# Performance work log

Measured on AMD Instinct MI355X. Metric: run time of the kernel, lower is better.

The kernel has to match this reference:

```python
import jax, jax.numpy as jnp
import numpy as np

B, T, E = 2, 2048, 1024
H, D = 16, 64
FF = 4096
EPS = 1e-5


def _layer_norm(x, g, b):
    m = jnp.mean(x, axis=-1, keepdims=True)
    v = jnp.mean(jnp.square(x - m), axis=-1, keepdims=True)
    return (x - m) * jax.lax.rsqrt(v + EPS) * g + b


def setup_inputs() -> dict:
    key = jax.random.key(0)
    ks = jax.random.split(key, 8)
    s = lambda fan_in: 1.0 / np.sqrt(fan_in)
    return {
        "src": jax.random.normal(ks[0], (B, T, E), jnp.float32),
        "Wq": jax.random.normal(ks[1], (E, E), jnp.float32) * s(E),
        "Wk": jax.random.normal(ks[2], (E, E), jnp.float32) * s(E),
        "Wv": jax.random.normal(ks[3], (E, E), jnp.float32) * s(E),
        "Wo": jax.random.normal(ks[4], (E, E), jnp.float32) * s(E),
        "W1": jax.random.normal(ks[5], (2 * FF, E), jnp.float32) * s(E),
        "b1": jnp.zeros((2 * FF,), jnp.float32),
        "W2": jax.random.normal(ks[6], (E, FF), jnp.float32) * s(FF),
        "b2": jnp.zeros((E,), jnp.float32),
        "ln1_w": jnp.ones((E,), jnp.float32),
        "ln1_b": jnp.zeros((E,), jnp.float32),
        "ln2_w": jnp.ones((E,), jnp.float32),
        "ln2_b": jnp.zeros((E,), jnp.float32),
    }


def reference(src, Wq, Wk, Wv, Wo, W1, b1, W2, b2, ln1_w, ln1_b, ln2_w, ln2_b):
    # --- pre-norm self-attention block ---
    h = _layer_norm(src, ln1_w, ln1_b)                       # [B,T,E]
    q = (h @ Wq.T).reshape(B, T, H, D)                       # [B,T,H,D]
    k = (h @ Wk.T).reshape(B, T, H, D)
    v = (h @ Wv.T).reshape(B, T, H, D)
    scores = jnp.einsum("bqhd,bkhd->bhqk", q, k) / np.sqrt(D)
    probs = jax.nn.softmax(scores, axis=-1)                  # [B,H,T,T]
    attn = jnp.einsum("bhqk,bkhd->bqhd", probs, v).reshape(B, T, E)
    x = src + attn @ Wo.T                                    # residual (dropout=0)
    # --- pre-norm GEGLU FFN block ---
    h2 = _layer_norm(x, ln2_w, ln2_b)
    u = h2 @ W1.T + b1                                       # [B,T,2*FF]
    a, gates = jnp.split(u, 2, axis=-1)
    f = a * jax.nn.gelu(gates, approximate=False)            # GEGLU (exact erf gelu)
    return x + (f @ W2.T + b2)
```

## Files before the change

### kernel.cpp

```cpp
#include <hip/hip_runtime.h>
#include <stdint.h>
#include <math.h>

#define DEVI __device__ __forceinline__

typedef __attribute__((ext_vector_type(8))) short sv8;
typedef __attribute__((ext_vector_type(4))) short sv4;
typedef __attribute__((ext_vector_type(4))) float fv4;

typedef __attribute__((address_space(1))) void av1_t;
typedef __attribute__((address_space(3))) void av3_t;

constexpr int Bb = 2, Tt = 2048, Ee = 1024, Hh = 16, Dd = 64, FFd = 4096;
constexpr int NN = Bb * Tt;
constexpr float EPSv = 1e-5f;

#define WAIT_VM(n) asm volatile("s_waitcnt vmcnt(" #n ")" ::: "memory")
#define LGKM0 asm volatile("s_waitcnt lgkmcnt(0)" ::: "memory")

DEVI float b2f(unsigned short s) {
  union { unsigned u; float f; } v; v.u = ((unsigned)s) << 16; return v.f;
}
DEVI unsigned short f2b(float f) {
  union { float f; unsigned u; } v; v.f = f;
  return (unsigned short)((v.u + 0x7FFFu + ((v.u >> 16) & 1u)) >> 16);
}
DEVI unsigned short f2b_rtz(float f) {
  union { float f; unsigned u; } v; v.f = f;
  return (unsigned short)(v.u >> 16);
}

DEVI void load_lds16(const void* g, void* s) {
  __builtin_amdgcn_global_load_lds((av1_t*)(unsigned long long)g,
                                   (av3_t*)(unsigned)(unsigned long long)s,
                                   16, 0, 0);
}

__global__ __launch_bounds__(256) void cvt_all_kernel(
    const float* __restrict__ Wq, const float* __restrict__ Wk,
    const float* __restrict__ Wv, const float* __restrict__ Wo,
    const float* __restrict__ W1, const float* __restrict__ W2,
    unsigned short* __restrict__ wqkv, unsigned short* __restrict__ wo16,
    unsigned short* __restrict__ w116, unsigned short* __restrict__ w216,
    float s2) {
  const int bid = blockIdx.x;
  if (bid < 4096) {
    const int wsel = bid >> 10;
    const int i = ((bid & 1023) * 256 + threadIdx.x) * 4;
    const float* src = (wsel == 0) ? Wq : (wsel == 1) ? Wk : (wsel == 2) ? Wv : Wo;
    unsigned short* dst = (wsel == 3) ? wo16 : (wqkv + (size_t)wsel * Ee * Ee);
    const float sc = (wsel == 0) ? s2 : 1.0f;
    const float4 v = *(const float4*)(src + i);
    sv4 o;
    o[0] = (short)f2b(v.x * sc); o[1] = (short)f2b(v.y * sc);
    o[2] = (short)f2b(v.z * sc); o[3] = (short)f2b(v.w * sc);
    *(sv4*)(dst + i) = o;
  } else if (bid < 12288) {
    const int i = ((bid - 4096) * 256 + threadIdx.x) * 4;
    const int r = i >> 10, c = i & 1023;
    const int rp = (r < FFd) ? ((r >> 4) * 32 + (r & 15))
                             : (((r - FFd) >> 4) * 32 + 16 + (r & 15));
    const float4 v = *(const float4*)(W1 + i);
    sv4 o;
    o[0] = (short)f2b(v.x); o[1] = (short)f2b(v.y);
    o[2] = (short)f2b(v.z); o[3] = (short)f2b(v.w);
    *(sv4*)(w116 + (size_t)rp * Ee + c) = o;
  } else {
    const int i = ((bid - 12288) * 256 + threadIdx.x) * 4;
    const float4 v = *(const float4*)(W2 + i);
    sv4 o;
    o[0] = (short)f2b(v.x); o[1] = (short)f2b(v.y);
    o[2] = (short)f2b(v.z); o[3] = (short)f2b(v.w);
    *(sv4*)(w216 + i) = o;
  }
}

__global__ __launch_bounds__(256) void vt_kernel(const unsigned short* __restrict__ qkv,
                                                 unsigned short* __restrict__ vT) {
  const int bh = blockIdx.y;
  const int b = bh >> 4, h = bh & 15;
  const int tt = blockIdx.x * 64;
  const int tid = threadIdx.x;
  __shared__ unsigned short tile[64][65];
  const int tr = tid >> 2, tc4 = (tid & 3) * 16;
  const unsigned short* src = qkv + (size_t)(b * Tt + tt + tr) * (3 * Ee) + 2 * Ee + h * 64 + tc4;
  const sv8 a0 = *(const sv8*)src;
  const sv8 a1 = *(const sv8*)(src + 8);
#pragma unroll
  for (int j = 0; j < 8; ++j) { tile[tr][tc4 + j] = a0[j]; tile[tr][tc4 + 8 + j] = a1[j]; }
  __syncthreads();
  unsigned short* dst = vT + ((size_t)bh * 64 + tr) * Tt + tt + tc4;
  sv8 o0, o1;
#pragma unroll
  for (int j = 0; j < 8; ++j) { o0[j] = (short)tile[tc4 + j][tr]; o1[j] = (short)tile[tc4 + 8 + j][tr]; }
  *(sv8*)dst = o0;
  *(sv8*)(dst + 8) = o1;
}

__global__ __launch_bounds__(256) void ln_kernel(const float* __restrict__ x,
                                                 const float* __restrict__ g,
                                                 const float* __restrict__ b,
                                                 unsigned short* __restrict__ out) {
  const int row = blockIdx.x, tid = threadIdx.x;
  const float4 v = *(const float4*)(x + (size_t)row * Ee + tid * 4);
  float s = v.x + v.y + v.z + v.w;
  float ss = v.x * v.x + v.y * v.y + v.z * v.z + v.w * v.w;
#pragma unroll
  for (int off = 32; off; off >>= 1) { s += __shfl_down(s, off); ss += __shfl_down(ss, off); }
  __shared__ float red[16];
  const int w = tid >> 6, l = tid & 63;
  if (l == 0) { red[w] = s; red[8 + w] = ss; }
  __syncthreads();
  s = red[0] + red[1] + red[2] + red[3];
  ss = red[8] + red[9] + red[10] + red[11];
  const float mean = s * (1.f / Ee);
  const float rstd = rsqrtf(ss * (1.f / Ee) - mean * mean + EPSv);
  const float4 gv = *(const float4*)(g + tid * 4);
  const float4 bv = *(const float4*)(b + tid * 4);
  sv4 o;
  o[0] = (short)f2b((v.x - mean) * rstd * gv.x + bv.x);
  o[1] = (short)f2b((v.y - mean) * rstd * gv.y + bv.y);
  o[2] = (short)f2b((v.z - mean) * rstd * gv.z + bv.z);
  o[3] = (short)f2b((v.w - mean) * rstd * gv.w + bv.w);
  *(sv4*)(out + (size_t)row * Ee + tid * 4) = o;
}

template <int OUTF32, int HASBIAS, int BN, int GEGLU>
__global__ __launch_bounds__(256) void gemm_bt(const unsigned short* __restrict__ A,
                                               const unsigned short* __restrict__ Bw,
                                               void* __restrict__ Cout,
                                               const float* __restrict__ bias,
                                               const float* __restrict__ res,
                                               int M, int K) {
  constexpr int NI = BN / 32;
  __shared__ unsigned short lA[3][128 * 32];
  __shared__ unsigned short lB[3][BN * 32];
  const int tid = threadIdx.x;
  const int l = tid & 63, w = tid >> 6;
  const int wr = w >> 1, wc = w & 1;
  const int rowbase = blockIdx.y * 128, colbase = blockIdx.x * BN;

  const fv4 zero4 = {0.f, 0.f, 0.f, 0.f};
  fv4 acc[4][NI];
#pragma unroll
  for (int i = 0; i < 4; ++i)
#pragma unroll
    for (int j = 0; j < NI; ++j) acc[i][j] = zero4;

  const int c0 = tid, c1 = tid + 256;
  const int sw0 = ((c0 & 3) ^ ((c0 >> 3) & 3)) * 8;
  const int sw1 = ((c1 & 3) ^ ((c1 >> 3) & 3)) * 8;
  const unsigned short* Ag0 = A + (size_t)(rowbase + (c0 >> 2)) * K + sw0;
  const unsigned short* Ag1 = A + (size_t)(rowbase + (c1 >> 2)) * K + sw1;
  const unsigned short* Bg0 = Bw + (size_t)(colbase + (c0 >> 2)) * K + sw0;
  const unsigned short* Bg1 = Bw + (size_t)(colbase + ((BN == 128 ? c1 : c0) >> 2)) * K +
                              (BN == 128 ? sw1 : sw0);

  const int nk = K >> 5;

  auto stage = [&](int buf) {
    load_lds16(Ag0, lA[buf] + c0 * 8);
    load_lds16(Ag1, lA[buf] + c1 * 8);
    load_lds16(Bg0, lB[buf] + c0 * 8);
    if (BN == 128) load_lds16(Bg1, lB[buf] + c1 * 8);
    Ag0 += 32; Ag1 += 32; Bg0 += 32; Bg1 += 32;
  };

  stage(0);
  stage(1);
  if constexpr (BN == 128) WAIT_VM(4); else WAIT_VM(3);
  __builtin_amdgcn_s_barrier();

  int cur = 0;
  for (int t = 0; t < nk; ++t) {
    const int pf = (cur + 2 >= 3) ? cur - 1 : cur + 2;
    if (t + 2 < nk) stage(pf);
    sv8 af[4], bfr[NI];
#pragma unroll
    for (int i = 0; i < 4; ++i) {
      const int ra = wr * 64 + i * 16 + (l & 15);
      af[i] = *(const sv8*)(lA[cur] + ra * 32 + (((l >> 4) ^ ((ra >> 1) & 3)) * 8));
    }
#pragma unroll
    for (int i = 0; i < NI; ++i) {
      const int rb = wc * (BN / 2) + i * 16 + (l & 15);
      bfr[i] = *(const sv8*)(lB[cur] + rb * 32 + (((l >> 4) ^ ((rb >> 1) & 3)) * 8));
    }
    __builtin_amdgcn_s_setprio(1);
#pragma unroll
    for (int mi = 0; mi < 4; ++mi)
#pragma unroll
      for (int ni = 0; ni < NI; ++ni)
        acc[mi][ni] = __builtin_amdgcn_mfma_f32_16x16x32_bf16(af[mi], bfr[ni], acc[mi][ni], 0, 0, 0);
    __builtin_amdgcn_s_setprio(0);
    if (t + 2 < nk) {
      if constexpr (BN == 128) WAIT_VM(4); else WAIT_VM(3);
      __builtin_amdgcn_s_barrier();
    } else if (t + 1 < nk) {
      WAIT_VM(0);
      __builtin_amdgcn_s_barrier();
    }
    cur = (cur + 1 >= 3) ? 0 : cur + 1;
  }

  const int r0 = rowbase + wr * 64 + ((l >> 4) * 4);
  const int ccol = colbase + wc * (BN / 2) + (l & 15);
#pragma unroll
  for (int mi = 0; mi < 4; ++mi) {
#pragma unroll
    for (int j = 0; j < 4; ++j) {
      const size_t r = (size_t)(r0 + mi * 16 + j);
      if (GEGLU) {
#pragma unroll
        for (int p = 0; p < NI / 2; ++p) {
          const int ca = ccol + p * 32;
          const int ocol = ((ca >> 5) << 4) | (ca & 15);
          const float av = acc[mi][2 * p][j] + bias[ocol];
          const float gv = acc[mi][2 * p + 1][j] + bias[ocol + (M >> 1)];
          const float y = 0.7978845608028654f * (gv + 0.044715f * gv * gv * gv);
          const float e = exp2f(2.8853900817779268f * y);
          const float gel = gv * (1.f - 1.f / (e + 1.f));
          ((unsigned short*)Cout)[r * (size_t)(M >> 1) + ocol] = f2b(av * gel);
        }
      } else {
#pragma unroll
        for (int ni = 0; ni < NI; ++ni) {
          const int c = ccol + ni * 16;
          float vv = acc[mi][ni][j];
          if (HASBIAS) vv += bias[c];
          if (OUTF32) {
            ((float*)Cout)[r * M + c] = res[r * M + c] + vv;
          } else {
            ((unsigned short*)Cout)[r * M + c] = f2b(vv);
          }
        }
      }
    }
  }
}

template <int GEGLU>
__global__ __launch_bounds__(512, 2) void gemm256(const unsigned short* __restrict__ A,
                                                  const unsigned short* __restrict__ Bw,
                                                  void* __restrict__ Cout,
                                                  const float* __restrict__ bias,
                                                  int M, int K) {
  __shared__ unsigned short Ah[2][2][256 * 32];
  __shared__ unsigned short Bh[2][2][256 * 32];
  const int tid = threadIdx.x;
  const int l = tid & 63, w = tid >> 6;
  const int wrow = w >> 2, wcol = w & 3;
  const int nbase = blockIdx.y * 256, mbase = blockIdx.x * 256;

  const fv4 zero4 = {0.f, 0.f, 0.f, 0.f};
  fv4 acc[8][4];
#pragma unroll
  for (int i = 0; i < 8; ++i)
#pragma unroll
    for (int j = 0; j < 4; ++j) acc[i][j] = zero4;

  const int s0 = tid, s1 = tid + 512;
  const int r0 = s0 >> 2, x0 = (((s0 & 3) ^ ((r0 >> 1) & 3))) * 8;
  const int r1 = s1 >> 2, x1 = (((s1 & 3) ^ ((r1 >> 1) & 3))) * 8;
  const unsigned short* As0 = A + (size_t)(nbase + r0) * K + x0;
  const unsigned short* As1 = A + (size_t)(nbase + r1) * K + x1;
  const unsigned short* Bs0 = Bw + (size_t)(mbase + r0) * K + x0;
  const unsigned short* Bs1 = Bw + (size_t)(mbase + r1) * K + x1;

  const int nk = K >> 6;

  auto stA = [&](int db, int kh, int kof) {
    load_lds16(As0 + kof + kh * 32, &Ah[db][kh][s0 * 8]);
    load_lds16(As1 + kof + kh * 32, &Ah[db][kh][s1 * 8]);
  };
  auto stB = [&](int db, int kh, int kof) {
    load_lds16(Bs0 + kof + kh * 32, &Bh[db][kh][s0 * 8]);
    load_lds16(Bs1 + kof + kh * 32, &Bh[db][kh][s1 * 8]);
  };

  const int cl = (((l >> 4) ^ ((l >> 1) & 3))) * 8;
  const int arl = (wrow * 128 + (l & 15)) * 32 + cl;
  const int brl = (wcol * 64 + (l & 15)) * 32 + cl;

  stA(0, 0, 0); stB(0, 0, 0); stA(0, 1, 0); stB(0, 1, 0);

  for (int t = 0; t < nk; ++t) {
    const int st = t & 1, sf = st ^ 1;
    const int kof = (t + 1) * 64;
    const bool pre = (t + 1 < nk);
    sv8 af[8], b0, b1;

    WAIT_VM(4);
    __builtin_amdgcn_s_barrier();
    __builtin_amdgcn_sched_barrier(0);
    if (pre) stA(sf, 0, kof);
#pragma unroll
    for (int mi = 0; mi < 8; ++mi) af[mi] = *(const sv8*)(&Ah[st][0][arl + mi * 512]);
    b0 = *(const sv8*)(&Bh[st][0][brl]);
    b1 = *(const sv8*)(&Bh[st][0][brl + 512]);
    __builtin_amdgcn_s_setprio(1);
#pragma unroll
    for (int mi = 0; mi < 8; ++mi) {
      acc[mi][0] = __builtin_amdgcn_mfma_f32_16x16x32_bf16(af[mi], b0, acc[mi][0], 0, 0, 0);
      acc[mi][1] = __builtin_amdgcn_mfma_f32_16x16x32_bf16(af[mi], b1, acc[mi][1], 0, 0, 0);
    }
    __builtin_amdgcn_s_setprio(0);

    if (pre) stB(sf, 0, kof);
    b0 = *(const sv8*)(&Bh[st][0][brl + 2 * 512]);
    b1 = *(const sv8*)(&Bh[st][0][brl + 3 * 512]);
    __builtin_amdgcn_s_setprio(1);
#pragma unroll
    for (int mi = 0; mi < 8; ++mi) {
      acc[mi][2] = __builtin_amdgcn_mfma_f32_16x16x32_bf16(af[mi], b0, acc[mi][2], 0, 0, 0);
      acc[mi][3] = __builtin_amdgcn_mfma_f32_16x16x32_bf16(af[mi], b1, acc[mi][3], 0, 0, 0);
    }
    __builtin_amdgcn_s_setprio(0);

    if (pre) { WAIT_VM(4); } else { WAIT_VM(0); }
    __builtin_amdgcn_s_barrier();
    __builtin_amdgcn_sched_barrier(0);
    if (pre) stA(sf, 1, kof);
#pragma unroll
    for (int mi = 0; mi < 8; ++mi) af[mi] = *(const sv8*)(&Ah[st][1][arl + mi * 512]);
    b0 = *(const sv8*)(&Bh[st][1][brl]);
    b1 = *(const sv8*)(&Bh[st][1][brl + 512]);
    __builtin_amdgcn_s_setprio(1);
#pragma unroll
    for (int mi = 0; mi < 8; ++mi) {
      acc[mi][0] = __builtin_amdgcn_mfma_f32_16x16x32_bf16(af[mi], b0, acc[mi][0], 0, 0, 0);
      acc[mi][1] = __builtin_amdgcn_mfma_f32_16x16x32_bf16(af[mi], b1, acc[mi][1], 0, 0, 0);
    }
    __builtin_amdgcn_s_setprio(0);

    if (pre) stB(sf, 1, kof);
    b0 = *(const sv8*)(&Bh[st][1][brl + 2 * 512]);
    b1 = *(const sv8*)(&Bh[st][1][brl + 3 * 512]);
    __builtin_amdgcn_s_setprio(1);
#pragma unroll
    for (int mi = 0; mi < 8; ++mi) {
      acc[mi][2] = __builtin_amdgcn_mfma_f32_16x16x32_bf16(af[mi], b0, acc[mi][2], 0, 0, 0);
      acc[mi][3] = __builtin_amdgcn_mfma_f32_16x16x32_bf16(af[mi], b1, acc[mi][3], 0, 0, 0);
    }
    __builtin_amdgcn_s_setprio(0);
  }

  const int rbase = nbase + wrow * 128 + ((l >> 4) * 4);
  const int cbase = mbase + wcol * 64 + (l & 15);
#pragma unroll
  for (int mi = 0; mi < 8; ++mi) {
#pragma unroll
    for (int j = 0; j < 4; ++j) {
      const size_t r = (size_t)(rbase + mi * 16 + j);
      if (GEGLU) {
#pragma unroll
        for (int p = 0; p < 2; ++p) {
          const int ca = cbase + p * 32;
          const int ocol = ((ca >> 5) << 4) | (ca & 15);
          const float av = acc[mi][2 * p][j] + bias[ocol];
          const float gv = acc[mi][2 * p + 1][j] + bias[ocol + (M >> 1)];
          const float y = 0.7978845608028654f * (gv + 0.044715f * gv * gv * gv);
          const float e = exp2f(2.8853900817779268f * y);
          const float gel = gv * (1.f - 1.f / (e + 1.f));
          ((unsigned short*)Cout)[r * (size_t)(M >> 1) + ocol] = f2b(av * gel);
        }
      } else {
#pragma unroll
        for (int ni = 0; ni < 4; ++ni) {
          const int c = cbase + ni * 16;
          ((unsigned short*)Cout)[r * (size_t)M + c] = f2b(acc[mi][ni][j]);
        }
      }
    }
  }
}

__global__ __launch_bounds__(256) void attn_kernel(const unsigned short* __restrict__ Q,
                                                   const unsigned short* __restrict__ Kb,
                                                   const unsigned short* __restrict__ vT,
                                                   unsigned short* __restrict__ O,
                                                   int ld) {
  const int bidl = ((blockIdx.x & 7) << 7) + (blockIdx.x >> 3);
  const int bh = bidl >> 5;
  const int b = bh / Hh, h = bh % Hh;
  const int q0 = (bidl & 31) * 64;
  const int tid = threadIdx.x, l = tid & 63, w = tid >> 6;
  const size_t base = (size_t)b * Tt * ld + (size_t)h * Dd;
  const size_t baseO = (size_t)b * Tt * Ee + (size_t)h * Dd;
  const unsigned short* vTb = vT + (size_t)bh * 64 * Tt;

  __shared__ unsigned short Kt[2][64 * 64];
  __shared__ unsigned short Vt[2][64 * 64];
  __shared__ unsigned short Pt[4][16 * 64];

  sv8 qf0, qf1;
  {
    const unsigned short* qp = Q + base + (size_t)(q0 + w * 16 + (l & 15)) * ld + (l >> 4) * 8;
    qf0 = *(const sv8*)qp;
    qf1 = *(const sv8*)(qp + 32);
  }

  const fv4 zero4 = {0.f, 0.f, 0.f, 0.f};
  fv4 acc_o[4];
#pragma unroll
  for (int i = 0; i < 4; ++i) acc_o[i] = zero4;
  float Mx = -INFINITY;
  float Lp[4];
#pragma unroll
  for (int j = 0; j < 4; ++j) Lp[j] = 0.f;

  const int c0 = tid, c1 = tid + 256;
  const int r0c = c0 >> 3, xc0 = c0 & 7;
  const int r1c = c1 >> 3, xc1 = c1 & 7;

  load_lds16(Kb + base + (size_t)(r0c)*ld + (xc0 ^ (r0c & 7)) * 8, Kt[0] + c0 * 8);
  load_lds16(Kb + base + (size_t)(r1c)*ld + (xc1 ^ (r1c & 7)) * 8, Kt[0] + c1 * 8);
  load_lds16(vTb + (size_t)(r0c)*Tt + (xc0 ^ (r0c & 7)) * 8, Vt[0] + c0 * 8);
  load_lds16(vTb + (size_t)(r1c)*Tt + (xc1 ^ (r1c & 7)) * 8, Vt[0] + c1 * 8);
  __syncthreads();

  int cur = 0;
  for (int kt = 0; kt < Tt / 64; ++kt) {
    const int nx = cur ^ 1;
    if (kt + 1 < Tt / 64) {
      load_lds16(Kb + base + (size_t)((kt + 1) * 64 + r0c) * ld + (xc0 ^ (r0c & 7)) * 8, Kt[nx] + c0 * 8);
      load_lds16(Kb + base + (size_t)((kt + 1) * 64 + r1c) * ld + (xc1 ^ (r1c & 7)) * 8, Kt[nx] + c1 * 8);
      load_lds16(vTb + (size_t)(r0c)*Tt + (kt + 1) * 64 + (xc0 ^ (r0c & 7)) * 8, Vt[nx] + c0 * 8);
      load_lds16(vTb + (size_t)(r1c)*Tt + (kt + 1) * 64 + (xc1 ^ (r1c & 7)) * 8, Vt[nx] + c1 * 8);
    }

    fv4 s[4];
    __builtin_amdgcn_s_setprio(1);
#pragma unroll
    for (int ks = 0; ks < 4; ++ks) {
      const int row = ks * 16 + (l & 15);
      const sv8 kf0 = *(const sv8*)(Kt[cur] + row * 64 + (((l >> 4) ^ (row & 7)) * 8));
      const sv8 kf1 = *(const sv8*)(Kt[cur] + row * 64 + (((4 + (l >> 4)) ^ (row & 7)) * 8));
      fv4 t = zero4;
      t = __builtin_amdgcn_mfma_f32_16x16x32_bf16(qf0, kf0, t, 0, 0, 0);
      t = __builtin_amdgcn_mfma_f32_16x16x32_bf16(qf1, kf1, t, 0, 0, 0);
      s[ks] = t;
    }
    __builtin_amdgcn_s_setprio(0);

    float m01 = fmaxf(fmaxf(s[0][0], s[0][1]), fmaxf(s[0][2], s[0][3]));
    float m1 = fmaxf(fmaxf(s[1][0], s[1][1]), fmaxf(s[1][2], s[1][3]));
    float m2 = fmaxf(fmaxf(s[2][0], s[2][1]), fmaxf(s[2][2], s[2][3]));
    float m3 = fmaxf(fmaxf(s[3][0], s[3][1]), fmaxf(s[3][2], s[3][3]));
    float tm = fmaxf(fmaxf(m01, m1), fmaxf(m2, m3));
    if (__any(tm > Mx + 11.5f)) {
      float mt = tm;
#pragma unroll
      for (int off = 1; off < 16; off <<= 1) mt = fmaxf(mt, __shfl_xor(mt, off, 16));
      const float mnew = fmaxf(Mx, mt);
      const float alpha = exp2f(Mx - mnew);
      Mx = mnew;
#pragma unroll
      for (int j = 0; j < 4; ++j) {
        Lp[j] *= alpha;
#pragma unroll
        for (int dsb = 0; dsb < 4; ++dsb) acc_o[dsb][j] *= alpha;
      }
    }
#pragma unroll
    for (int ks = 0; ks < 4; ++ks)
#pragma unroll
      for (int j = 0; j < 4; ++j) {
        const float p = exp2f(s[ks][j] - Mx);
        s[ks][j] = p;
        Lp[j] += p;
      }
#pragma unroll
    for (int ks = 0; ks < 4; ++ks)
#pragma unroll
      for (int j = 0; j < 4; ++j) {
        const int q = (l >> 4) * 4 + j, k = ks * 16 + (l & 15);
        Pt[w][q * 64 + ((((k >> 3) ^ (q & 7)) & 7) * 8) + (k & 7)] = f2b_rtz(s[ks][j]);
      }
    LGKM0;

    __builtin_amdgcn_s_setprio(1);
#pragma unroll
    for (int kcn = 0; kcn < 2; ++kcn) {
      const int qr = l & 15;
      const sv8 pf = *(const sv8*)(&Pt[w][qr * 64 + (((kcn * 4 + (l >> 4)) ^ (qr & 7)) * 8)]);
#pragma unroll
      for (int dsb = 0; dsb < 4; ++dsb) {
        const int row = dsb * 16 + (l & 15);
        const int chunk = kcn * 4 + (l >> 4);
        const sv8 vf = *(const sv8*)(Vt[cur] + row * 64 + ((chunk ^ (row & 7)) * 8));
        acc_o[dsb] = __builtin_amdgcn_mfma_f32_16x16x32_bf16(pf, vf, acc_o[dsb], 0, 0, 0);
      }
    }
    __builtin_amdgcn_s_setprio(0);

    __syncthreads();
    cur = nx;
  }

#pragma unroll
  for (int j = 0; j < 4; ++j) {
    float t = Lp[j];
#pragma unroll
    for (int off = 1; off < 16; off <<= 1) t += __shfl_xor(t, off, 16);
    const float inv = 1.f / t;
    unsigned short* op = O + baseO + (size_t)(q0 + w * 16 + (l >> 4) * 4 + j) * Ee;
#pragma unroll
    for (int dsb = 0; dsb < 4; ++dsb)
      op[dsb * 16 + (l & 15)] = f2b(acc_o[dsb][j] * inv);
  }
}

extern "C" void kernel_launch(void* const* d_in, const int* in_sizes, int n_in,
                              void* d_out, int out_size, void* d_ws, size_t ws_size,
                              hipStream_t stream) {
  (void)in_sizes; (void)n_in; (void)out_size; (void)ws_size;
  const float* src  = (const float*)d_in[0];
  const float* Wq   = (const float*)d_in[1];
  const float* Wk   = (const float*)d_in[2];
  const float* Wv   = (const float*)d_in[3];
  const float* Wo   = (const float*)d_in[4];
  const float* W1   = (const float*)d_in[5];
  const float* b1   = (const float*)d_in[6];
  const float* W2   = (const float*)d_in[7];
  const float* b2   = (const float*)d_in[8];
  const float* ln1w = (const float*)d_in[9];
  const float* ln1b = (const float*)d_in[10];
  const float* ln2w = (const float*)d_in[11];
  const float* ln2b = (const float*)d_in[12];
  float* out = (float*)d_out;

  char* ws = (char*)d_ws;
  size_t off = 0;
  auto alloc = [&](size_t bytes) { char* p = ws + off; off += bytes; return p; };
  unsigned short* wqkv = (unsigned short*)alloc((size_t)3 * Ee * Ee * 2);
  unsigned short* wo16 = (unsigned short*)alloc((size_t)Ee * Ee * 2);
  unsigned short* w116 = (unsigned short*)alloc((size_t)2 * FFd * Ee * 2);
  unsigned short* w216 = (unsigned short*)alloc((size_t)Ee * FFd * 2);
  unsigned short* h16  = (unsigned short*)alloc((size_t)NN * Ee * 2);
  unsigned short* qkv  = (unsigned short*)alloc((size_t)NN * 3 * Ee * 2);
  unsigned short* a16  = (unsigned short*)alloc((size_t)NN * Ee * 2);
  float* xbuf          = (float*)alloc((size_t)NN * Ee * 4);
  unsigned short* vT   = (unsigned short*)alloc((size_t)NN * Ee * 2);
  unsigned short* f16  = qkv;

  const float s2 = 0.125f * 1.4426950408889634f;

  dim3 blk(256);
  cvt_all_kernel<<<dim3(16384), blk, 0, stream>>>(Wq, Wk, Wv, Wo, W1, W2,
                                                  wqkv, wo16, w116, w216, s2);

  ln_kernel<<<dim3(NN), blk, 0, stream>>>(src, ln1w, ln1b, h16);

  gemm_bt<0, 0, 128, 0><<<dim3(3 * Ee / 128, NN / 128), blk, 0, stream>>>(h16, wqkv, qkv, nullptr, nullptr, 3 * Ee, Ee);

  vt_kernel<<<dim3(Tt / 64, Bb * Hh), blk, 0, stream>>>(qkv, vT);

  attn_kernel<<<dim3(1024), blk, 0, stream>>>(qkv, qkv + Ee, vT, a16, 3 * Ee);

  gemm_bt<1, 0, 64, 0><<<dim3(Ee / 64, NN / 128), blk, 0, stream>>>(a16, wo16, xbuf, nullptr, src, Ee, Ee);

  ln_kernel<<<dim3(NN), blk, 0, stream>>>(xbuf, ln2w, ln2b, h16);

  gemm256<1><<<dim3(2 * FFd / 256, NN / 256), dim3(512), 0, stream>>>(h16, w116, f16, b1, 2 * FFd, Ee);

  gemm_bt<1, 1, 64, 0><<<dim3(Ee / 64, NN / 128), blk, 0, stream>>>(f16, w216, out, b2, xbuf, Ee, FFd);
}
```

Before: 292.5 us.

## Shrink GEGLU GEMM tile to 256x128 with triple-buffered 32-wide K pipeline

```diff
diff --git a/kernel.cpp b/kernel.cpp
--- a/kernel.cpp
+++ b/kernel.cpp
@@ -240,64 +240,58 @@
 }
 
 template <int GEGLU>
-__global__ __launch_bounds__(512, 2) void gemm256(const unsigned short* __restrict__ A,
+__global__ __launch_bounds__(512, 4) void gemm256(const unsigned short* __restrict__ A,
                                                   const unsigned short* __restrict__ Bw,
                                                   void* __restrict__ Cout,
                                                   const float* __restrict__ bias,
                                                   int M, int K) {
-  __shared__ unsigned short Ah[2][2][256 * 32];
-  __shared__ unsigned short Bh[2][2][256 * 32];
+  __shared__ unsigned short Ah[3][256 * 32];
+  __shared__ unsigned short Bh[3][128 * 32];
   const int tid = threadIdx.x;
   const int l = tid & 63, w = tid >> 6;
   const int wrow = w >> 2, wcol = w & 3;
-  const int nbase = blockIdx.y * 256, mbase = blockIdx.x * 256;
+  const int nbase = blockIdx.y * 256, mbase = blockIdx.x * 128;
 
   const fv4 zero4 = {0.f, 0.f, 0.f, 0.f};
-  fv4 acc[8][4];
-#pragma unroll
-  for (int i = 0; i < 8; ++i)
-#pragma unroll
-    for (int j = 0; j < 4; ++j) acc[i][j] = zero4;
-
-  const int s0 = tid, s1 = tid + 512;
-  const int r0 = s0 >> 2, x0 = (((s0 & 3) ^ ((r0 >> 1) & 3))) * 8;
-  const int r1 = s1 >> 2, x1 = (((s1 & 3) ^ ((r1 >> 1) & 3))) * 8;
-  const unsigned short* As0 = A + (size_t)(nbase + r0) * K + x0;
-  const unsigned short* As1 = A + (size_t)(nbase + r1) * K + x1;
-  const unsigned short* Bs0 = Bw + (size_t)(mbase + r0) * K + x0;
-  const unsigned short* Bs1 = Bw + (size_t)(mbase + r1) * K + x1;
-
-  const int nk = K >> 6;
-
-  auto stA = [&](int db, int kh, int kof) {
-    load_lds16(As0 + kof + kh * 32, &Ah[db][kh][s0 * 8]);
-    load_lds16(As1 + kof + kh * 32, &Ah[db][kh][s1 * 8]);
-  };
-  auto stB = [&](int db, int kh, int kof) {
-    load_lds16(Bs0 + kof + kh * 32, &Bh[db][kh][s0 * 8]);
-    load_lds16(Bs1 + kof + kh * 32, &Bh[db][kh][s1 * 8]);
+  fv4 acc[8][2];
+#pragma unroll
+  for (int i = 0; i < 8; ++i) { acc[i][0] = zero4; acc[i][1] = zero4; }
+
+  const int sA0 = tid, sA1 = tid + 512;
+  const int rA0 = sA0 >> 2, xA0 = ((sA0 & 3) ^ ((rA0 >> 1) & 3)) * 8;
+  const int rA1 = sA1 >> 2, xA1 = ((sA1 & 3) ^ ((rA1 >> 1) & 3)) * 8;
+  const int rB = tid >> 2, xB = ((tid & 3) ^ ((rB >> 1) & 3)) * 8;
+  const unsigned short* As0 = A + (size_t)(nbase + rA0) * K + xA0;
+  const unsigned short* As1 = A + (size_t)(nbase + rA1) * K + xA1;
+  const unsigned short* Bs = Bw + (size_t)(mbase + rB) * K + xB;
+
+  const int nk = K >> 5;
+
+  auto stage = [&](int buf, int kof) {
+    load_lds16(As0 + kof, &Ah[buf][sA0 * 8]);
+    load_lds16(As1 + kof, &Ah[buf][sA1 * 8]);
+    load_lds16(Bs + kof, &Bh[buf][tid * 8]);
   };
 
   const int cl = (((l >> 4) ^ ((l >> 1) & 3))) * 8;
   const int arl = (wrow * 128 + (l & 15)) * 32 + cl;
-  const int brl = (wcol * 64 + (l & 15)) * 32 + cl;
-
-  stA(0, 0, 0); stB(0, 0, 0); stA(0, 1, 0); stB(0, 1, 0);
-
+  const int brl = (wcol * 32 + (l & 15)) * 32 + cl;
+
+  stage(0, 0);
+  stage(1, 32);
+
+  int cur = 0;
   for (int t = 0; t < nk; ++t) {
-    const int st = t & 1, sf = st ^ 1;
-    const int kof = (t + 1) * 64;
-    const bool pre = (t + 1 < nk);
-    sv8 af[8], b0, b1;
-
-    WAIT_VM(4);
+    if (t + 1 < nk) { WAIT_VM(3); } else { WAIT_VM(0); }
     __builtin_amdgcn_s_barrier();
     __builtin_amdgcn_sched_barrier(0);
-    if (pre) stA(sf, 0, kof);
-#pragma unroll
-    for (int mi = 0; mi < 8; ++mi) af[mi] = *(const sv8*)(&Ah[st][0][arl + mi * 512]);
-    b0 = *(const sv8*)(&Bh[st][0][brl]);
-    b1 = *(const sv8*)(&Bh[st][0][brl + 512]);
+    const int pf = (cur + 2 >= 3) ? cur - 1 : cur + 2;
+    if (t + 2 < nk) stage(pf, (t + 2) * 32);
+    sv8 af[8], b0, b1;
+#pragma unroll
+    for (int mi = 0; mi < 8; ++mi) af[mi] = *(const sv8*)(&Ah[cur][arl + mi * 512]);
+    b0 = *(const sv8*)(&Bh[cur][brl]);
+    b1 = *(const sv8*)(&Bh[cur][brl + 512]);
     __builtin_amdgcn_s_setprio(1);
 #pragma unroll
     for (int mi = 0; mi < 8; ++mi) {
@@ -305,68 +299,28 @@
       acc[mi][1] = __builtin_amdgcn_mfma_f32_16x16x32_bf16(af[mi], b1, acc[mi][1], 0, 0, 0);
     }
     __builtin_amdgcn_s_setprio(0);
-
-    if (pre) stB(sf, 0, kof);
-    b0 = *(const sv8*)(&Bh[st][0][brl + 2 * 512]);
-    b1 = *(const sv8*)(&Bh[st][0][brl + 3 * 512]);
-    __builtin_amdgcn_s_setprio(1);
-#pragma unroll
-    for (int mi = 0; mi < 8; ++mi) {
-      acc[mi][2] = __builtin_amdgcn_mfma_f32_16x16x32_bf16(af[mi], b0, acc[mi][2], 0, 0, 0);
-      acc[mi][3] = __builtin_amdgcn_mfma_f32_16x16x32_bf16(af[mi], b1, acc[mi][3], 0, 0, 0);
-    }
-    __builtin_amdgcn_s_setprio(0);
-
-    if (pre) { WAIT_VM(4); } else { WAIT_VM(0); }
-    __builtin_amdgcn_s_barrier();
-    __builtin_amdgcn_sched_barrier(0);
-    if (pre) stA(sf, 1, kof);
-#pragma unroll
-    for (int mi = 0; mi < 8; ++mi) af[mi] = *(const sv8*)(&Ah[st][1][arl + mi * 512]);
-    b0 = *(const sv8*)(&Bh[st][1][brl]);
-    b1 = *(const sv8*)(&Bh[st][1][brl + 512]);
-    __builtin_amdgcn_s_setprio(1);
-#pragma unroll
-    for (int mi = 0; mi < 8; ++mi) {
-      acc[mi][0] = __builtin_amdgcn_mfma_f32_16x16x32_bf16(af[mi], b0, acc[mi][0], 0, 0, 0);
-      acc[mi][1] = __builtin_amdgcn_mfma_f32_16x16x32_bf16(af[mi], b1, acc[mi][1], 0, 0, 0);
-    }
-    __builtin_amdgcn_s_setprio(0);
-
-    if (pre) stB(sf, 1, kof);
-    b0 = *(const sv8*)(&Bh[st][1][brl + 2 * 512]);
-    b1 = *(const sv8*)(&Bh[st][1][brl + 3 * 512]);
-    __builtin_amdgcn_s_setprio(1);
-#pragma unroll
-    for (int mi = 0; mi < 8; ++mi) {
-      acc[mi][2] = __builtin_amdgcn_mfma_f32_16x16x32_bf16(af[mi], b0, acc[mi][2], 0, 0, 0);
-      acc[mi][3] = __builtin_amdgcn_mfma_f32_16x16x32_bf16(af[mi], b1, acc[mi][3], 0, 0, 0);
-    }
-    __builtin_amdgcn_s_setprio(0);
+    cur = (cur + 1 >= 3) ? 0 : cur + 1;
   }
 
   const int rbase = nbase + wrow * 128 + ((l >> 4) * 4);
-  const int cbase = mbase + wcol * 64 + (l & 15);
+  const int cbase = mbase + wcol * 32 + (l & 15);
 #pragma unroll
   for (int mi = 0; mi < 8; ++mi) {
 #pragma unroll
     for (int j = 0; j < 4; ++j) {
       const size_t r = (size_t)(rbase + mi * 16 + j);
       if (GEGLU) {
-#pragma unroll
-        for (int p = 0; p < 2; ++p) {
-          const int ca = cbase + p * 32;
-          const int ocol = ((ca >> 5) << 4) | (ca & 15);
-          const float av = acc[mi][2 * p][j] + bias[ocol];
-          const float gv = acc[mi][2 * p + 1][j] + bias[ocol + (M >> 1)];
-          const float y = 0.7978845608028654f * (gv + 0.044715f * gv * gv * gv);
-          const float e = exp2f(2.8853900817779268f * y);
-          const float gel = gv * (1.f - 1.f / (e + 1.f));
-          ((unsigned short*)Cout)[r * (size_t)(M >> 1) + ocol] = f2b(av * gel);
-        }
+        const int ca = cbase;
+        const int ocol = ((ca >> 5) << 4) | (ca & 15);
+        const float av = acc[mi][0][j] + bias[ocol];
+        const float gv = acc[mi][1][j] + bias[ocol + (M >> 1)];
+        const float y = 0.7978845608028654f * (gv + 0.044715f * gv * gv * gv);
+        const float e = exp2f(2.8853900817779268f * y);
+        const float gel = gv * (1.f - 1.f / (e + 1.f));
+        ((unsigned short*)Cout)[r * (size_t)(M >> 1) + ocol] = f2b(av * gel);
       } else {
 #pragma unroll
-        for (int ni = 0; ni < 4; ++ni) {
+        for (int ni = 0; ni < 2; ++ni) {
           const int c = cbase + ni * 16;
           ((unsigned short*)Cout)[r * (size_t)M + c] = f2b(acc[mi][ni][j]);
         }
@@ -562,7 +516,7 @@
 
   ln_kernel<<<dim3(NN), blk, 0, stream>>>(xbuf, ln2w, ln2b, h16);
 
-  gemm256<1><<<dim3(2 * FFd / 256, NN / 256), dim3(512), 0, stream>>>(h16, w116, f16, b1, 2 * FFd, Ee);
+  gemm256<1><<<dim3(2 * FFd / 128, NN / 256), dim3(512), 0, stream>>>(h16, w116, f16, b1, 2 * FFd, Ee);
 
   gemm_bt<1, 1, 64, 0><<<dim3(Ee / 64, NN / 128), blk, 0, stream>>>(f16, w216, out, b2, xbuf, Ee, FFd);
 }
```

Result: no change. 296.0 us (+1.2%).
